# Kernel tuning notes

Hardware: AMD Instinct MI355X
Metric: run time of the kernel (lower is better)

Reference implementation:

```python
import jax, jax.numpy as jnp
import numpy as np

NUM_GRAPHS = 16
MAX_NODES = 256
EMB_DIM = 64
EDGES_PER_GRAPH = 4096


def setup_inputs() -> dict:
    rng = np.random.default_rng(0)
    src_list, dst_list = [], []
    for g in range(NUM_GRAPHS):
        # distinct off-diagonal (src,dst) pairs per graph (simple directed graph, no self loops)
        flat = rng.choice(MAX_NODES * MAX_NODES, size=EDGES_PER_GRAPH + MAX_NODES, replace=False)
        s, d = flat // MAX_NODES, flat % MAX_NODES
        keep = s != d
        s, d = s[keep][:EDGES_PER_GRAPH], d[keep][:EDGES_PER_GRAPH]
        off = g * MAX_NODES
        src_list.append(s + off)
        dst_list.append(d + off)
    edge_index = jnp.asarray(
        np.stack([np.concatenate(src_list), np.concatenate(dst_list)]), dtype=jnp.int32)
    batch_vec = jnp.repeat(jnp.arange(NUM_GRAPHS, dtype=jnp.int32), MAX_NODES)
    k1, k2 = jax.random.split(jax.random.key(0))
    edge_attr = jax.random.normal(k1, (NUM_GRAPHS * EDGES_PER_GRAPH, EMB_DIM), jnp.float32)
    emb_table = jax.random.normal(k2, (3, EMB_DIM), jnp.float32)
    return {"edge_attr": edge_attr, "emb_table": emb_table,
            "edge_index": edge_index, "batch_vec": batch_vec}


def reference(edge_attr, emb_table, edge_index, batch_vec):
    B, N, D = NUM_GRAPHS, MAX_NODES, edge_attr.shape[-1]
    # per-graph node offsets (pyG-style, from the batch vector)
    counts = jax.ops.segment_sum(jnp.ones_like(batch_vec), batch_vec, num_segments=B)
    starts = jnp.cumsum(counts) - counts  # first global node index of each graph
    src, dst = edge_index[0], edge_index[1]
    g = batch_vec[src]
    ls = src - starts[g]  # local row index
    ld = dst - starts[g]  # local col index
    # to_dense_adj with edge_attr: scatter-add edge features -> [B, N, N, D]
    edge_dense = jnp.zeros((B, N, N, D), edge_attr.dtype).at[g, ls, ld].add(edge_attr)
    # edge types: scatter 2 at edges, add_self_loops fill 1 on the diagonal
    t = jnp.zeros((B, N, N), jnp.int32).at[g, ls, ld].add(2)
    node = jnp.arange(batch_vec.shape[0], dtype=jnp.int32)
    gn = batch_vec
    ln = node - starts[gn]
    t = t.at[gn, ln, ln].add(1)
    A = 2 - t  # 0 = connected, 1 = diagonal, 2 = disconnected/padding
    table = emb_table.at[0].set(0.0)  # padding_idx=0 -> zero vector for connected pairs
    return edge_dense + table[A]
```

## Files before the change

### kernel.cpp

```cpp
#include <hip/hip_runtime.h>

#define NB 16
#define NN 256
#define ND 64
#define NE (16*4096)
#define NNODE (NB*NN)
#define MASK_WORDS (NNODE*8)

#define EDGE_BLOCKS 4096
#define FILL_BLOCKS NNODE

typedef float f4 __attribute__((ext_vector_type(4)));

__global__ __launch_bounds__(256) void mask_kernel(const int* __restrict__ edge_index,
                                                   unsigned* __restrict__ mask) {
    const int e = blockIdx.x * 256 + threadIdx.x;
    if (e >= NE) return;
    const int src = edge_index[e];
    const int ld  = edge_index[NE + e] & (NN - 1);
    atomicOr(&mask[src * 8 + (ld >> 5)], 1u << (ld & 31));
}

__global__ __launch_bounds__(256) void fused_kernel(const float* __restrict__ edge_attr,
                                                    const int* __restrict__ edge_index,
                                                    const float* __restrict__ emb,
                                                    const unsigned* __restrict__ mask,
                                                    f4* __restrict__ out) {
    if (blockIdx.x < EDGE_BLOCKS) {
        const int t = blockIdx.x * 256 + threadIdx.x;
        const int e = t >> 4;
        const int q = t & 15;
        const int src = edge_index[e];
        const int ld  = edge_index[NE + e] & (NN - 1);
        out[((long)src * NN + ld) * (ND / 4) + q] =
            ((const f4*)edge_attr)[(long)e * (ND / 4) + q];
        return;
    }

    const int row  = blockIdx.x - EDGE_BLOCKS;
    const int diag = row & (NN - 1);
    const unsigned* __restrict__ mrow = mask + row * 8;
    unsigned w[8];
    #pragma unroll
    for (int k = 0; k < 8; ++k) w[k] = mrow[k];

    const int ci = threadIdx.x >> 4;
    const int dq = threadIdx.x & 15;
    const f4 v1 = ((const f4*)(emb + 1 * ND))[dq];
    const f4 v2 = ((const f4*)(emb + 2 * ND))[dq];
    f4* __restrict__ rowout = out + (long)row * NN * (ND / 4);

    #pragma unroll
    for (int pass = 0; pass < 16; ++pass) {
        const int col = pass * 16 + ci;
        const unsigned bits = w[pass >> 1] >> ((pass & 1) * 16);
        if (!((bits >> ci) & 1u)) {
            rowout[col * (ND / 4) + dq] = (col == diag) ? v1 : v2;
        }
    }
}

extern "C" void kernel_launch(void* const* d_in, const int* in_sizes, int n_in,
                              void* d_out, int out_size, void* d_ws, size_t ws_size,
                              hipStream_t stream) {
    const float* edge_attr  = (const float*)d_in[0];
    const float* emb_table  = (const float*)d_in[1];
    const int*   edge_index = (const int*)d_in[2];
    f4*       out  = (f4*)d_out;
    unsigned* mask = (unsigned*)d_ws;

    hipMemsetAsync(mask, 0, MASK_WORDS * sizeof(unsigned), stream);
    mask_kernel<<<NE / 256, 256, 0, stream>>>(edge_index, mask);
    fused_kernel<<<EDGE_BLOCKS + FILL_BLOCKS, 256, 0, stream>>>(
        edge_attr, edge_index, emb_table, mask, out);
}
```

Baseline: 58.62 us.

## Fuse mask build, fill and edge scatter into one per-row kernel

Replaces the memset, the global-atomic mask kernel and the split fused kernel with a single kernel that gives each output row its own block. Each block scans its graph's 4096 source indices, builds the row's adjacency mask and edge list in shared memory, writes the embedding fill for non-edge columns, then copies the edge features for that row's edges. This removes two launches, the workspace round trip and the global atomics. In exchange every block re-reads 16KB of src indices, 256 times per graph, and edge copies are serialized per row. It also assumes a row never has more than 256 edges.

```diff
diff --git a/kernel.cpp b/kernel.cpp
--- a/kernel.cpp
+++ b/kernel.cpp
@@ -3,60 +3,69 @@
 #define NB 16
 #define NN 256
 #define ND 64
-#define NE (16*4096)
-#define NNODE (NB*NN)
-#define MASK_WORDS (NNODE*8)
-
-#define EDGE_BLOCKS 4096
-#define FILL_BLOCKS NNODE
+#define EPG 4096
+#define NE (NB*EPG)
+#define MAXE_ROW 256
 
 typedef float f4 __attribute__((ext_vector_type(4)));
+typedef int   i4 __attribute__((ext_vector_type(4)));
 
-__global__ __launch_bounds__(256) void mask_kernel(const int* __restrict__ edge_index,
-                                                   unsigned* __restrict__ mask) {
-    const int e = blockIdx.x * 256 + threadIdx.x;
-    if (e >= NE) return;
-    const int src = edge_index[e];
-    const int ld  = edge_index[NE + e] & (NN - 1);
-    atomicOr(&mask[src * 8 + (ld >> 5)], 1u << (ld & 31));
-}
+__global__ __launch_bounds__(256) void row_kernel(const float* __restrict__ edge_attr,
+                                                  const int* __restrict__ edge_index,
+                                                  const float* __restrict__ emb,
+                                                  f4* __restrict__ out) {
+    __shared__ unsigned lmask[8];
+    __shared__ int      lcnt;
+    __shared__ int      llist[MAXE_ROW];
+    const int row = blockIdx.x;
+    const int g   = row >> 8;
+    const int tid = threadIdx.x;
 
-__global__ __launch_bounds__(256) void fused_kernel(const float* __restrict__ edge_attr,
-                                                    const int* __restrict__ edge_index,
-                                                    const float* __restrict__ emb,
-                                                    const unsigned* __restrict__ mask,
-                                                    f4* __restrict__ out) {
-    if (blockIdx.x < EDGE_BLOCKS) {
-        const int t = blockIdx.x * 256 + threadIdx.x;
-        const int e = t >> 4;
-        const int q = t & 15;
-        const int src = edge_index[e];
-        const int ld  = edge_index[NE + e] & (NN - 1);
-        out[((long)src * NN + ld) * (ND / 4) + q] =
-            ((const f4*)edge_attr)[(long)e * (ND / 4) + q];
-        return;
+    if (tid < 8) lmask[tid] = 0u;
+    if (tid == 0) lcnt = 0;
+    __syncthreads();
+
+    const i4* __restrict__ srcv = (const i4*)(edge_index + g * EPG);
+    #pragma unroll
+    for (int k = 0; k < 4; ++k) {
+        const int vi = tid + k * 256;
+        const i4 s = srcv[vi];
+        #pragma unroll
+        for (int j = 0; j < 4; ++j) {
+            if (s[j] == row) {
+                const int e  = g * EPG + vi * 4 + j;
+                const int ld = edge_index[NE + e] & (NN - 1);
+                atomicOr(&lmask[ld >> 5], 1u << (ld & 31));
+                const int p = atomicAdd(&lcnt, 1);
+                llist[p] = (e << 8) | ld;
+            }
+        }
     }
+    __syncthreads();
 
-    const int row  = blockIdx.x - EDGE_BLOCKS;
+    const int ci = tid >> 4;
+    const int dq = tid & 15;
+    const f4 v1 = ((const f4*)(emb + 1 * ND))[dq];
+    const f4 v2 = ((const f4*)(emb + 2 * ND))[dq];
     const int diag = row & (NN - 1);
-    const unsigned* __restrict__ mrow = mask + row * 8;
+    f4* __restrict__ rowout = out + (long)row * NN * (ND / 4);
     unsigned w[8];
     #pragma unroll
-    for (int k = 0; k < 8; ++k) w[k] = mrow[k];
-
-    const int ci = threadIdx.x >> 4;
-    const int dq = threadIdx.x & 15;
-    const f4 v1 = ((const f4*)(emb + 1 * ND))[dq];
-    const f4 v2 = ((const f4*)(emb + 2 * ND))[dq];
-    f4* __restrict__ rowout = out + (long)row * NN * (ND / 4);
-
+    for (int k = 0; k < 8; ++k) w[k] = lmask[k];
     #pragma unroll
     for (int pass = 0; pass < 16; ++pass) {
         const int col = pass * 16 + ci;
         const unsigned bits = w[pass >> 1] >> ((pass & 1) * 16);
-        if (!((bits >> ci) & 1u)) {
+        if (!((bits >> ci) & 1u))
             rowout[col * (ND / 4) + dq] = (col == diag) ? v1 : v2;
-        }
+    }
+
+    const int cnt = lcnt;
+    for (int k = tid >> 4; k < cnt; k += 16) {
+        const int pk = llist[k];
+        const int e  = pk >> 8;
+        const int ld = pk & 255;
+        rowout[ld * (ND / 4) + dq] = ((const f4*)edge_attr)[(long)e * (ND / 4) + dq];
     }
 }
 
@@ -66,11 +75,7 @@
     const float* edge_attr  = (const float*)d_in[0];
     const float* emb_table  = (const float*)d_in[1];
     const int*   edge_index = (const int*)d_in[2];
-    f4*       out  = (f4*)d_out;
-    unsigned* mask = (unsigned*)d_ws;
+    f4* out = (f4*)d_out;
 
-    hipMemsetAsync(mask, 0, MASK_WORDS * sizeof(unsigned), stream);
-    mask_kernel<<<NE / 256, 256, 0, stream>>>(edge_index, mask);
-    fused_kernel<<<EDGE_BLOCKS + FILL_BLOCKS, 256, 0, stream>>>(
-        edge_attr, edge_index, emb_table, mask, out);
+    row_kernel<<<NB * NN, 256, 0, stream>>>(edge_attr, edge_index, emb_table, out);
 }
```

Result: no change. 58.99 us (+0.6%).
